# Kernel optimization log

Hardware: AMD Instinct MI355X
Metric: run time of the kernel (lower is better)

Reference implementation:

```python
import jax, jax.numpy as jnp
import numpy as np

N = 50000      # nodes
E = 800000     # directed edges (avg degree 16)
IN = 96
H = 96
OUT = 96


def _gcn(x, W, b, src, dst, norm, n):
    # PyG GCNConv: h = x @ W; aggregate norm * h[src] at dst; add bias.
    h = x @ W                          # [N, H]
    msg = h[src] * norm[:, None]       # [E+N, H]
    out = jax.ops.segment_sum(msg, dst, num_segments=n)
    return out + b


def setup_inputs() -> dict:
    key = jax.random.key(0)
    ks = jax.random.split(key, 12)
    s = 1.0 / np.sqrt(IN)
    sh = 1.0 / np.sqrt(H)
    return {
        "x": jax.random.normal(ks[0], (N, IN), dtype=jnp.float32),
        "edge_index": jax.random.randint(ks[1], (2, E), 0, N, dtype=jnp.int32),
        "W_local": jax.random.uniform(ks[2], (IN, H), jnp.float32, -s, s),
        "b_local": jnp.zeros((H,), jnp.float32),
        "W_g1": jax.random.uniform(ks[3], (IN, H), jnp.float32, -s, s),
        "b_g1": jnp.zeros((H,), jnp.float32),
        "W_g2": jax.random.uniform(ks[4], (H, H), jnp.float32, -sh, sh),
        "b_g2": jnp.zeros((H,), jnp.float32),
        "W_fuse": jax.random.uniform(ks[5], (2 * H, OUT), jnp.float32, -1.0 / np.sqrt(2 * H), 1.0 / np.sqrt(2 * H)),
        "b_fuse": jnp.zeros((OUT,), jnp.float32),
    }


def reference(x, edge_index, W_local, b_local, W_g1, b_g1, W_g2, b_g2, W_fuse, b_fuse):
    n = x.shape[0]
    loops = jnp.arange(n, dtype=edge_index.dtype)
    src = jnp.concatenate([edge_index[0], loops])   # add self-loops (GCNConv default)
    dst = jnp.concatenate([edge_index[1], loops])
    deg = jax.ops.segment_sum(jnp.ones_like(dst, dtype=x.dtype), dst, num_segments=n)
    dis = jax.lax.rsqrt(jnp.maximum(deg, 1.0))      # deg >= 1 due to self-loops
    norm = dis[src] * dis[dst]                      # sym-normalized edge weights

    local = jax.nn.relu(_gcn(x, W_local, b_local, src, dst, norm, n))
    g = jax.nn.relu(_gcn(x, W_g1, b_g1, src, dst, norm, n))
    g = jax.nn.relu(_gcn(g, W_g2, b_g2, src, dst, norm, n))

    combined = jnp.concatenate([local, g], axis=-1)  # [N, 2H]
    return combined @ W_fuse + b_fuse                # [N, OUT]
```

## Files before the change

### kernel.cpp

```cpp
#include <hip/hip_runtime.h>

#define HDIM 96
#define LSTR 104

typedef __attribute__((ext_vector_type(8))) short bf16x8;
typedef __attribute__((ext_vector_type(4))) float f32x4;

#define LGKM0() do { asm volatile("s_waitcnt lgkmcnt(0)" ::: "memory"); \
                     __builtin_amdgcn_sched_barrier(0); } while (0)

__device__ __forceinline__ unsigned short bf16rne(float x) {
  const unsigned u = __float_as_uint(x);
  return (unsigned short)((u + 0x7fff + ((u >> 16) & 1)) >> 16);
}

__device__ __forceinline__ void split2(float x, unsigned short& hi, unsigned short& lo) {
  const unsigned u = __float_as_uint(x);
  hi = (unsigned short)(u >> 16);
  const float xhi = __uint_as_float(u & 0xffff0000u);
  lo = (unsigned short)(__float_as_uint(x - xhi) >> 16);
}

__global__ void zero_k(int* __restrict__ p, int n) {
  int i = blockIdx.x * blockDim.x + threadIdx.x;
  if (i < n) p[i] = 0;
}

__global__ void deg_rank_k(const int* __restrict__ dst, int* __restrict__ indeg,
                           int* __restrict__ rank, int e) {
  int i = blockIdx.x * blockDim.x + threadIdx.x;
  if (i < e) rank[i] = atomicAdd(&indeg[dst[i]], 1);
}

__device__ __forceinline__ int wave_incl_scan(int v, int lane) {
#pragma unroll
  for (int off = 1; off < 64; off <<= 1) {
    int t = __shfl_up(v, off, 64);
    if (lane >= off) v += t;
  }
  return v;
}

__global__ __launch_bounds__(1024) void scan_a_split_k(
    const int* __restrict__ indeg, int* __restrict__ bsum, int n, int nb,
    const float* __restrict__ W0, const float* __restrict__ W1,
    const float* __restrict__ W2, const float* __restrict__ W3,
    unsigned short* __restrict__ dH, unsigned short* __restrict__ dL) {
  const int tid = threadIdx.x;
  if (blockIdx.x >= nb) {
    const int t = (blockIdx.x - nb) * 1024 + tid;
    if (t < 5 * 9216) {
      const int tile = t / 9216, r = t % 9216;
      const int nn = r / 96, k = r % 96;
      const float* W = (tile == 0) ? W0 : (tile == 1) ? W1 : (tile == 2) ? W2 : W3;
      const int row = (tile == 4) ? 96 + k : k;
      unsigned short h, l;
      split2(W[row * 96 + nn], h, l);
      dH[t] = h;
      dL[t] = l;
    }
    return;
  }
  __shared__ int ws[16];
  const int i = blockIdx.x * 1024 + tid;
  int v = (i < n) ? indeg[i] : 0;
#pragma unroll
  for (int off = 32; off; off >>= 1) v += __shfl_down(v, off, 64);
  if ((tid & 63) == 0) ws[tid >> 6] = v;
  __syncthreads();
  if (tid < 16) {
    int s = ws[tid];
#pragma unroll
    for (int off = 8; off; off >>= 1) s += __shfl_down(s, off, 16);
    if (tid == 0) bsum[blockIdx.x] = s;
  }
}

__global__ __launch_bounds__(1024) void scan_b_k(const int* __restrict__ bsum,
                                                 int* __restrict__ bbase,
                                                 int* __restrict__ offsets, int nb, int n) {
  __shared__ int ws[16];
  const int tid = threadIdx.x, lane = tid & 63, w = tid >> 6;
  const int v = (tid < nb) ? bsum[tid] : 0;
  int incl = wave_incl_scan(v, lane);
  if (lane == 63) ws[w] = incl;
  __syncthreads();
  if (tid < 16) {
    int s = ws[tid];
#pragma unroll
    for (int off = 1; off < 16; off <<= 1) {
      int t = __shfl_up(s, off, 16);
      if (tid >= off) s += t;
    }
    ws[tid] = s;
  }
  __syncthreads();
  incl += (w > 0 ? ws[w - 1] : 0);
  if (tid < nb) bbase[tid] = incl - v;
  if (tid == 0) offsets[n] = ws[15];
}

__global__ __launch_bounds__(1024) void scan_c_k(const int* __restrict__ indeg,
                                                 const int* __restrict__ bbase,
                                                 int* __restrict__ offsets,
                                                 float* __restrict__ dis, int n) {
  __shared__ int ws[16];
  const int tid = threadIdx.x, lane = tid & 63, w = tid >> 6;
  const int i = blockIdx.x * 1024 + tid;
  const int v = (i < n) ? indeg[i] : 0;
  int incl = wave_incl_scan(v, lane);
  if (lane == 63) ws[w] = incl;
  __syncthreads();
  if (tid < 16) {
    int s = ws[tid];
#pragma unroll
    for (int off = 1; off < 16; off <<= 1) {
      int t = __shfl_up(s, off, 16);
      if (tid >= off) s += t;
    }
    ws[tid] = s;
  }
  __syncthreads();
  incl += (w > 0 ? ws[w - 1] : 0);
  if (i < n) {
    offsets[i] = bbase[blockIdx.x] + incl - v;
    dis[i] = rsqrtf((float)(1 + v));
  }
}

__global__ __launch_bounds__(256) void place_scale_k(
    const int* __restrict__ src, const int* __restrict__ dst,
    const int* __restrict__ rank, const int* __restrict__ offsets,
    int* __restrict__ csr_src, int e, int pb,
    const float* __restrict__ x, const float* __restrict__ dis,
    unsigned short* __restrict__ o, int n) {
  if (blockIdx.x < pb) {
    int i = blockIdx.x * 256 + threadIdx.x;
    if (i >= e) return;
    int d = dst[i];
    atomicExch(&csr_src[offsets[d] + rank[i]], src[i]);
  } else {
    int t = (blockIdx.x - pb) * 256 + threadIdx.x;
    if (t >= n * 24) return;
    const float d = dis[t / 24];
    float4 v = ((const float4*)x)[t];
    ushort4 h;
    h.x = bf16rne(v.x * d); h.y = bf16rne(v.y * d);
    h.z = bf16rne(v.z * d); h.w = bf16rne(v.w * d);
    ((ushort4*)o)[t] = h;
  }
}

__device__ __forceinline__ void acc8(float* a, uint4 p) {
  a[0] += __uint_as_float(p.x << 16);
  a[1] += __uint_as_float(p.x & 0xffff0000u);
  a[2] += __uint_as_float(p.y << 16);
  a[3] += __uint_as_float(p.y & 0xffff0000u);
  a[4] += __uint_as_float(p.z << 16);
  a[5] += __uint_as_float(p.z & 0xffff0000u);
  a[6] += __uint_as_float(p.w << 16);
  a[7] += __uint_as_float(p.w & 0xffff0000u);
}

__device__ __forceinline__ void gather_x4p(const int* __restrict__ csr,
                                           int i, int end,
                                           const unsigned short* __restrict__ hp,
                                           int quad, float a[3][8]) {
  const int q8 = 8 * quad;
  int s0 = 0, s1 = 0, s2 = 0, s3 = 0;
  if (i + 3 < end) { s0 = csr[i]; s1 = csr[i + 1]; s2 = csr[i + 2]; s3 = csr[i + 3]; }
  while (i + 3 < end) {
    const unsigned short* p0 = hp + (size_t)s0 * HDIM + q8;
    const unsigned short* p1 = hp + (size_t)s1 * HDIM + q8;
    const unsigned short* p2 = hp + (size_t)s2 * HDIM + q8;
    const unsigned short* p3 = hp + (size_t)s3 * HDIM + q8;
    const uint4 v00 = *(const uint4*)(p0), v01 = *(const uint4*)(p0 + 32), v02 = *(const uint4*)(p0 + 64);
    const uint4 v10 = *(const uint4*)(p1), v11 = *(const uint4*)(p1 + 32), v12 = *(const uint4*)(p1 + 64);
    const uint4 v20 = *(const uint4*)(p2), v21 = *(const uint4*)(p2 + 32), v22 = *(const uint4*)(p2 + 64);
    const uint4 v30 = *(const uint4*)(p3), v31 = *(const uint4*)(p3 + 32), v32 = *(const uint4*)(p3 + 64);
    i += 4;
    if (i + 3 < end) { s0 = csr[i]; s1 = csr[i + 1]; s2 = csr[i + 2]; s3 = csr[i + 3]; }
    acc8(a[0], v00); acc8(a[1], v01); acc8(a[2], v02);
    acc8(a[0], v10); acc8(a[1], v11); acc8(a[2], v12);
    acc8(a[0], v20); acc8(a[1], v21); acc8(a[2], v22);
    acc8(a[0], v30); acc8(a[1], v31); acc8(a[2], v32);
  }
  for (; i < end; i++) {
    const unsigned short* p = hp + (size_t)csr[i] * HDIM + q8;
    acc8(a[0], *(const uint4*)p);
    acc8(a[1], *(const uint4*)(p + 32));
    acc8(a[2], *(const uint4*)(p + 64));
  }
}

__device__ __forceinline__ void flush_tile(const unsigned short* TB,
                                           unsigned short* __restrict__ g,
                                           int row0w, int M, int lane) {
  const int rr = lane >> 2, sb = lane & 3;
  const int grow = row0w + rr;
#pragma unroll
  for (int j = 0; j < 3; j++) {
    const int slot = sb + 4 * j;
    const uint4 v = *(const uint4*)(&TB[rr * LSTR + slot * 8]);
    if (grow < M) *(uint4*)(&g[(size_t)grow * HDIM + slot * 8]) = v;
  }
}

template<bool DUAL>
__global__ __launch_bounds__(256) void gat_gemm_k(
    const int* __restrict__ csr_src, const int* __restrict__ offsets,
    const float* __restrict__ dis, const unsigned short* __restrict__ hp,
    const unsigned short* __restrict__ WH0, const unsigned short* __restrict__ WL0,
    const float* __restrict__ b0,
    const unsigned short* __restrict__ WH1, const unsigned short* __restrict__ WL1,
    const float* __restrict__ b1,
    unsigned short* __restrict__ outH, unsigned short* __restrict__ outL,
    unsigned short* __restrict__ outMsg, int M) {
  __shared__ __align__(16) unsigned short Wh[96 * LSTR], Wl[96 * LSTR];
  __shared__ __align__(16) unsigned short TBUF[4][16 * LSTR];
  const int t = threadIdx.x;
  const int lane = t & 63, wv = t >> 6;
  const int m = lane & 15, quad = lane >> 4;
  const int row0 = blockIdx.x * 64;
  const int node = row0 + 16 * wv + m;
  unsigned short* TB = TBUF[wv];

  for (int u = t; u < 1152; u += 256) {
    const int nn = u / 12, kq = u % 12;
    *(uint4*)(&Wh[nn * LSTR + 8 * kq]) = ((const uint4*)(WH0 + (size_t)nn * HDIM))[kq];
    *(uint4*)(&Wl[nn * LSTR + 8 * kq]) = ((const uint4*)(WL0 + (size_t)nn * HDIM))[kq];
  }

  float a[3][8];
#pragma unroll
  for (int c = 0; c < 3; c++)
#pragma unroll
    for (int jj = 0; jj < 8; jj++) a[c][jj] = 0.f;
  if (node < M) {
    const float dd = dis[node];
    const int beg = offsets[node];
    const int end = offsets[node + 1];
    const unsigned short* selfp = hp + (size_t)node * HDIM + 8 * quad;
    const uint4 sv0 = *(const uint4*)(selfp);
    const uint4 sv1 = *(const uint4*)(selfp + 32);
    const uint4 sv2 = *(const uint4*)(selfp + 64);
    gather_x4p(csr_src, beg, end, hp, quad, a);
    acc8(a[0], sv0); acc8(a[1], sv1); acc8(a[2], sv2);
#pragma unroll
    for (int c = 0; c < 3; c++)
#pragma unroll
      for (int jj = 0; jj < 8; jj++) a[c][jj] *= dd;
  }
  bf16x8 ah[3], al[3];
#pragma unroll
  for (int c = 0; c < 3; c++)
#pragma unroll
    for (int jj = 0; jj < 8; jj++) {
      unsigned short h, l;
      split2(a[c][jj], h, l);
      ah[c][jj] = (short)h;
      al[c][jj] = (short)l;
    }

  __syncthreads();

  f32x4 acc0[6];
#pragma unroll
  for (int c = 0; c < 6; c++) acc0[c] = (f32x4){0.f, 0.f, 0.f, 0.f};
#pragma unroll
  for (int kc = 0; kc < 3; kc++) {
    const int ko = 32 * kc + 8 * quad;
#pragma unroll
    for (int c = 0; c < 6; c++) {
      const bf16x8 wh = *(const bf16x8*)(&Wh[(16 * c + m) * LSTR + ko]);
      const bf16x8 wl = *(const bf16x8*)(&Wl[(16 * c + m) * LSTR + ko]);
      acc0[c] = __builtin_amdgcn_mfma_f32_16x16x32_bf16(ah[kc], wh, acc0[c], 0, 0, 0);
      acc0[c] = __builtin_amdgcn_mfma_f32_16x16x32_bf16(ah[kc], wl, acc0[c], 0, 0, 0);
      acc0[c] = __builtin_amdgcn_mfma_f32_16x16x32_bf16(al[kc], wh, acc0[c], 0, 0, 0);
    }
  }

  const int row0w = row0 + 16 * wv;
#pragma unroll
  for (int c = 0; c < 6; c++) {
    const float bv = b0[16 * c + m];
#pragma unroll
    for (int r = 0; r < 4; r++) {
      const float v = fmaxf(acc0[c][r] + bv, 0.f);
      unsigned short h, l;
      split2(v, h, l);
      (void)l;
      TB[(4 * quad + r) * LSTR + 16 * c + m] = h;
    }
  }
  LGKM0();
  flush_tile(TB, outH, row0w, M, lane);
  LGKM0();
#pragma unroll
  for (int c = 0; c < 6; c++) {
    const float bv = b0[16 * c + m];
#pragma unroll
    for (int r = 0; r < 4; r++) {
      const float v = fmaxf(acc0[c][r] + bv, 0.f);
      unsigned short h, l;
      split2(v, h, l);
      (void)h;
      TB[(4 * quad + r) * LSTR + 16 * c + m] = l;
    }
  }
  LGKM0();
  flush_tile(TB, outL, row0w, M, lane);
  LGKM0();

  if (DUAL) {
    __syncthreads();
    for (int u = t; u < 1152; u += 256) {
      const int nn = u / 12, kq = u % 12;
      *(uint4*)(&Wh[nn * LSTR + 8 * kq]) = ((const uint4*)(WH1 + (size_t)nn * HDIM))[kq];
      *(uint4*)(&Wl[nn * LSTR + 8 * kq]) = ((const uint4*)(WL1 + (size_t)nn * HDIM))[kq];
    }
    __syncthreads();
    f32x4 acc1[6];
#pragma unroll
    for (int c = 0; c < 6; c++) acc1[c] = (f32x4){0.f, 0.f, 0.f, 0.f};
#pragma unroll
    for (int kc = 0; kc < 3; kc++) {
      const int ko = 32 * kc + 8 * quad;
#pragma unroll
      for (int c = 0; c < 6; c++) {
        const bf16x8 wh = *(const bf16x8*)(&Wh[(16 * c + m) * LSTR + ko]);
        const bf16x8 wl = *(const bf16x8*)(&Wl[(16 * c + m) * LSTR + ko]);
        acc1[c] = __builtin_amdgcn_mfma_f32_16x16x32_bf16(ah[kc], wh, acc1[c], 0, 0, 0);
        acc1[c] = __builtin_amdgcn_mfma_f32_16x16x32_bf16(ah[kc], wl, acc1[c], 0, 0, 0);
        acc1[c] = __builtin_amdgcn_mfma_f32_16x16x32_bf16(al[kc], wh, acc1[c], 0, 0, 0);
      }
    }
    float dv[4];
#pragma unroll
    for (int r = 0; r < 4; r++) dv[r] = (row0w + 4 * quad + r < M) ? dis[row0w + 4 * quad + r] : 0.f;
#pragma unroll
    for (int c = 0; c < 6; c++) {
      const float bv = b1[16 * c + m];
#pragma unroll
      for (int r = 0; r < 4; r++)
        TB[(4 * quad + r) * LSTR + 16 * c + m] =
            bf16rne(fmaxf(acc1[c][r] + bv, 0.f) * dv[r]);
    }
    LGKM0();
    flush_tile(TB, outMsg, row0w, M, lane);
  }
}

__global__ __launch_bounds__(256) void gemm_concat_k(
    const unsigned short* __restrict__ AH0, const unsigned short* __restrict__ AL0,
    const unsigned short* __restrict__ AH1, const unsigned short* __restrict__ AL1,
    const unsigned short* __restrict__ WH, const unsigned short* __restrict__ WL,
    const float* __restrict__ bias, float* __restrict__ out, int M) {
  __shared__ __align__(16) unsigned short Ah[64 * LSTR], Al[64 * LSTR];
  __shared__ __align__(16) unsigned short Wh[96 * LSTR], Wl[96 * LSTR];
  const int t = threadIdx.x;
  const int lane = t & 63, wv = t >> 6;
  const int m = lane & 15, quad = lane >> 4;
  const int row0 = blockIdx.x * 64;

  f32x4 acc[6];
#pragma unroll
  for (int c = 0; c < 6; c++) acc[c] = (f32x4){0.f, 0.f, 0.f, 0.f};

  for (int kt = 0; kt < 2; kt++) {
    const unsigned short* AH = kt ? AH1 : AH0;
    const unsigned short* AL = kt ? AL1 : AL0;
    if (kt) __syncthreads();
    for (int u = t; u < 768; u += 256) {
      const int r = u / 12, kq = u % 12;
      uint4 vh = make_uint4(0, 0, 0, 0), vl = make_uint4(0, 0, 0, 0);
      if (row0 + r < M) {
        vh = ((const uint4*)(AH + (size_t)(row0 + r) * HDIM))[kq];
        vl = ((const uint4*)(AL + (size_t)(row0 + r) * HDIM))[kq];
      }
      *(uint4*)(&Ah[r * LSTR + 8 * kq]) = vh;
      *(uint4*)(&Al[r * LSTR + 8 * kq]) = vl;
    }
    const unsigned short* WHt = WH + (size_t)kt * 9216;
    const unsigned short* WLt = WL + (size_t)kt * 9216;
    for (int u = t; u < 1152; u += 256) {
      const int nn = u / 12, kq = u % 12;
      *(uint4*)(&Wh[nn * LSTR + 8 * kq]) = ((const uint4*)(WHt + (size_t)nn * HDIM))[kq];
      *(uint4*)(&Wl[nn * LSTR + 8 * kq]) = ((const uint4*)(WLt + (size_t)nn * HDIM))[kq];
    }
    __syncthreads();
#pragma unroll
    for (int kc = 0; kc < 3; kc++) {
      const int ko = 32 * kc + 8 * quad;
      const bf16x8 ah = *(const bf16x8*)(&Ah[(16 * wv + m) * LSTR + ko]);
      const bf16x8 al = *(const bf16x8*)(&Al[(16 * wv + m) * LSTR + ko]);
#pragma unroll
      for (int c = 0; c < 6; c++) {
        const bf16x8 wh = *(const bf16x8*)(&Wh[(16 * c + m) * LSTR + ko]);
        const bf16x8 wl = *(const bf16x8*)(&Wl[(16 * c + m) * LSTR + ko]);
        acc[c] = __builtin_amdgcn_mfma_f32_16x16x32_bf16(ah, wh, acc[c], 0, 0, 0);
        acc[c] = __builtin_amdgcn_mfma_f32_16x16x32_bf16(ah, wl, acc[c], 0, 0, 0);
        acc[c] = __builtin_amdgcn_mfma_f32_16x16x32_bf16(al, wh, acc[c], 0, 0, 0);
      }
    }
  }

  float* TBf = (float*)(Ah + (size_t)(16 * wv) * LSTR);
  const int rr = lane >> 2, sb = lane & 3;
  const int grow = row0 + 16 * wv + rr;
  LGKM0();
#pragma unroll
  for (int half = 0; half < 2; half++) {
#pragma unroll
    for (int c = 0; c < 3; c++) {
      const int cc = 3 * half + c;
      const float bv = bias[16 * cc + m];
#pragma unroll
      for (int r = 0; r < 4; r++)
        TBf[(4 * quad + r) * 52 + 16 * c + m] = acc[cc][r] + bv;
    }
    LGKM0();
#pragma unroll
    for (int j = 0; j < 3; j++) {
      const int slot = sb + 4 * j;
      const float4 v = *(const float4*)(&TBf[rr * 52 + slot * 4]);
      if (grow < M) *(float4*)(&out[(size_t)grow * HDIM + half * 48 + slot * 4]) = v;
    }
    LGKM0();
  }
}

extern "C" void kernel_launch(void* const* d_in, const int* in_sizes, int n_in,
                              void* d_out, int out_size, void* d_ws, size_t ws_size,
                              hipStream_t stream) {
  const float* x       = (const float*)d_in[0];
  const int*   edge    = (const int*)d_in[1];
  const float* W_local = (const float*)d_in[2];
  const float* b_local = (const float*)d_in[3];
  const float* W_g1    = (const float*)d_in[4];
  const float* b_g1    = (const float*)d_in[5];
  const float* W_g2    = (const float*)d_in[6];
  const float* b_g2    = (const float*)d_in[7];
  const float* W_fuse  = (const float*)d_in[8];
  const float* b_fuse  = (const float*)d_in[9];
  float* out = (float*)d_out;

  const int n = in_sizes[0] / HDIM;
  const int e = in_sizes[1] / 2;
  const int* src = edge;
  const int* dst = edge + e;
  const int nb = (n + 1023) / 1024;

  char* ws = (char*)d_ws;
  auto alloc = [&](size_t bytes) { char* p = ws; ws += (bytes + 255) & ~(size_t)255; return p; };
  int*   indeg   = (int*)alloc((size_t)n * 4);
  float* dis     = (float*)alloc((size_t)n * 4);
  int*   offsets = (int*)alloc((size_t)(n + 1) * 4);
  int*   bsum    = (int*)alloc((size_t)nb * 4);
  int*   bbase   = (int*)alloc((size_t)nb * 4);
  int*   rank    = (int*)alloc((size_t)e * 4);
  int*   csr_src = (int*)alloc((size_t)e * 4);
  const size_t mat16 = (size_t)n * HDIM * 2;
  unsigned short* msgX = (unsigned short*)alloc(mat16);
  unsigned short* msgG = (unsigned short*)alloc(mat16);
  unsigned short* locH = (unsigned short*)alloc(mat16);
  unsigned short* locL = (unsigned short*)alloc(mat16);
  unsigned short* g2H  = (unsigned short*)alloc(mat16);
  unsigned short* g2L  = (unsigned short*)alloc(mat16);
  unsigned short* wH   = (unsigned short*)alloc(5 * 9216 * 2);
  unsigned short* wL   = (unsigned short*)alloc(5 * 9216 * 2);

  zero_k<<<(n + 255) / 256, 256, 0, stream>>>(indeg, n);
  deg_rank_k<<<(e + 255) / 256, 256, 0, stream>>>(dst, indeg, rank, e);
  scan_a_split_k<<<nb + 45, 1024, 0, stream>>>(indeg, bsum, n, nb,
                                               W_local, W_g1, W_g2, W_fuse, wH, wL);
  scan_b_k<<<1, 1024, 0, stream>>>(bsum, bbase, offsets, nb, n);
  scan_c_k<<<nb, 1024, 0, stream>>>(indeg, bbase, offsets, dis, n);
  const int pb = (e + 255) / 256;
  const int sb = (n * 24 + 255) / 256;
  place_scale_k<<<pb + sb, 256, 0, stream>>>(src, dst, rank, offsets, csr_src, e, pb,
                                             x, dis, msgX, n);

  const int gb = (n + 63) / 64;

  gat_gemm_k<true><<<gb, 256, 0, stream>>>(csr_src, offsets, dis, msgX,
                                           wH, wL, b_local,
                                           wH + 9216, wL + 9216, b_g1,
                                           locH, locL, msgG, n);
  gat_gemm_k<false><<<gb, 256, 0, stream>>>(csr_src, offsets, dis, msgG,
                                            wH + 2 * 9216, wL + 2 * 9216, b_g2,
                                            nullptr, nullptr, nullptr,
                                            g2H, g2L, nullptr, n);
  gemm_concat_k<<<gb, 256, 0, stream>>>(locH, locL, g2H, g2L,
                                        wH + 3 * 9216, wL + 3 * 9216, b_fuse, out, n);
}
```

Measured before the change: 262.9 us.

## Fuse final concat GEMM into second GCN aggregation kernel

The second gather+GEMM kernel now computes the fuse-layer GEMM directly. It reloads the local-branch activations (hi/lo bf16) per row and uses the just-computed g2 activations from registers via a shared-memory transpose. This removes the g2H/g2L intermediate write and read and one kernel launch. In exchange, each block reloads two more weight tiles into shared memory and needs extra syncs and more registers, which may lower occupancy.

```diff
diff --git a/kernel.cpp b/kernel.cpp
--- a/kernel.cpp
+++ b/kernel.cpp
@@ -206,7 +206,7 @@
   }
 }
 
-template<bool DUAL>
+template<bool DUAL, bool FUSE>
 __global__ __launch_bounds__(256) void gat_gemm_k(
     const int* __restrict__ csr_src, const int* __restrict__ offsets,
     const float* __restrict__ dis, const unsigned short* __restrict__ hp,
@@ -215,7 +215,10 @@
     const unsigned short* __restrict__ WH1, const unsigned short* __restrict__ WL1,
     const float* __restrict__ b1,
     unsigned short* __restrict__ outH, unsigned short* __restrict__ outL,
-    unsigned short* __restrict__ outMsg, int M) {
+    unsigned short* __restrict__ outMsg,
+    const unsigned short* __restrict__ WH2, const unsigned short* __restrict__ WL2,
+    const unsigned short* __restrict__ AH2, const unsigned short* __restrict__ AL2,
+    const float* __restrict__ bF, float* __restrict__ fout, int M) {
   __shared__ __align__(16) unsigned short Wh[96 * LSTR], Wl[96 * LSTR];
   __shared__ __align__(16) unsigned short TBUF[4][16 * LSTR];
   const int t = threadIdx.x;
@@ -262,6 +265,21 @@
       al[c][jj] = (short)l;
     }
 
+  bf16x8 lh[3], ll[3];
+  if (FUSE) {
+#pragma unroll
+    for (int kc = 0; kc < 3; kc++) { lh[kc] = (bf16x8){0,0,0,0,0,0,0,0}; ll[kc] = lh[kc]; }
+    if (node < M) {
+      const unsigned short* ph = AH2 + (size_t)node * HDIM + 8 * quad;
+      const unsigned short* pl = AL2 + (size_t)node * HDIM + 8 * quad;
+#pragma unroll
+      for (int kc = 0; kc < 3; kc++) {
+        lh[kc] = *(const bf16x8*)(ph + 32 * kc);
+        ll[kc] = *(const bf16x8*)(pl + 32 * kc);
+      }
+    }
+  }
+
   __syncthreads();
 
   f32x4 acc0[6];
@@ -281,36 +299,39 @@
   }
 
   const int row0w = row0 + 16 * wv;
-#pragma unroll
-  for (int c = 0; c < 6; c++) {
-    const float bv = b0[16 * c + m];
-#pragma unroll
-    for (int r = 0; r < 4; r++) {
-      const float v = fmaxf(acc0[c][r] + bv, 0.f);
-      unsigned short h, l;
-      split2(v, h, l);
-      (void)l;
-      TB[(4 * quad + r) * LSTR + 16 * c + m] = h;
-    }
-  }
-  LGKM0();
-  flush_tile(TB, outH, row0w, M, lane);
-  LGKM0();
-#pragma unroll
-  for (int c = 0; c < 6; c++) {
-    const float bv = b0[16 * c + m];
-#pragma unroll
-    for (int r = 0; r < 4; r++) {
-      const float v = fmaxf(acc0[c][r] + bv, 0.f);
-      unsigned short h, l;
-      split2(v, h, l);
-      (void)h;
-      TB[(4 * quad + r) * LSTR + 16 * c + m] = l;
-    }
-  }
-  LGKM0();
-  flush_tile(TB, outL, row0w, M, lane);
-  LGKM0();
+
+  if (!FUSE) {
+#pragma unroll
+    for (int c = 0; c < 6; c++) {
+      const float bv = b0[16 * c + m];
+#pragma unroll
+      for (int r = 0; r < 4; r++) {
+        const float v = fmaxf(acc0[c][r] + bv, 0.f);
+        unsigned short h, l;
+        split2(v, h, l);
+        (void)l;
+        TB[(4 * quad + r) * LSTR + 16 * c + m] = h;
+      }
+    }
+    LGKM0();
+    flush_tile(TB, outH, row0w, M, lane);
+    LGKM0();
+#pragma unroll
+    for (int c = 0; c < 6; c++) {
+      const float bv = b0[16 * c + m];
+#pragma unroll
+      for (int r = 0; r < 4; r++) {
+        const float v = fmaxf(acc0[c][r] + bv, 0.f);
+        unsigned short h, l;
+        split2(v, h, l);
+        (void)h;
+        TB[(4 * quad + r) * LSTR + 16 * c + m] = l;
+      }
+    }
+    LGKM0();
+    flush_tile(TB, outL, row0w, M, lane);
+    LGKM0();
+  }
 
   if (DUAL) {
     __syncthreads();
@@ -349,84 +370,109 @@
     LGKM0();
     flush_tile(TB, outMsg, row0w, M, lane);
   }
-}
-
-__global__ __launch_bounds__(256) void gemm_concat_k(
-    const unsigned short* __restrict__ AH0, const unsigned short* __restrict__ AL0,
-    const unsigned short* __restrict__ AH1, const unsigned short* __restrict__ AL1,
-    const unsigned short* __restrict__ WH, const unsigned short* __restrict__ WL,
-    const float* __restrict__ bias, float* __restrict__ out, int M) {
-  __shared__ __align__(16) unsigned short Ah[64 * LSTR], Al[64 * LSTR];
-  __shared__ __align__(16) unsigned short Wh[96 * LSTR], Wl[96 * LSTR];
-  const int t = threadIdx.x;
-  const int lane = t & 63, wv = t >> 6;
-  const int m = lane & 15, quad = lane >> 4;
-  const int row0 = blockIdx.x * 64;
-
-  f32x4 acc[6];
-#pragma unroll
-  for (int c = 0; c < 6; c++) acc[c] = (f32x4){0.f, 0.f, 0.f, 0.f};
-
-  for (int kt = 0; kt < 2; kt++) {
-    const unsigned short* AH = kt ? AH1 : AH0;
-    const unsigned short* AL = kt ? AL1 : AL0;
-    if (kt) __syncthreads();
-    for (int u = t; u < 768; u += 256) {
-      const int r = u / 12, kq = u % 12;
-      uint4 vh = make_uint4(0, 0, 0, 0), vl = make_uint4(0, 0, 0, 0);
-      if (row0 + r < M) {
-        vh = ((const uint4*)(AH + (size_t)(row0 + r) * HDIM))[kq];
-        vl = ((const uint4*)(AL + (size_t)(row0 + r) * HDIM))[kq];
-      }
-      *(uint4*)(&Ah[r * LSTR + 8 * kq]) = vh;
-      *(uint4*)(&Al[r * LSTR + 8 * kq]) = vl;
-    }
-    const unsigned short* WHt = WH + (size_t)kt * 9216;
-    const unsigned short* WLt = WL + (size_t)kt * 9216;
+
+  if (FUSE) {
+    bf16x8 gh[3], gl[3];
+#pragma unroll
+    for (int c = 0; c < 6; c++) {
+      const float bv = b0[16 * c + m];
+#pragma unroll
+      for (int r = 0; r < 4; r++) {
+        const float v = fmaxf(acc0[c][r] + bv, 0.f);
+        unsigned short h, l;
+        split2(v, h, l);
+        (void)l;
+        TB[(4 * quad + r) * LSTR + 16 * c + m] = h;
+      }
+    }
+    LGKM0();
+#pragma unroll
+    for (int kc = 0; kc < 3; kc++)
+      gh[kc] = *(const bf16x8*)(&TB[m * LSTR + 32 * kc + 8 * quad]);
+    LGKM0();
+#pragma unroll
+    for (int c = 0; c < 6; c++) {
+      const float bv = b0[16 * c + m];
+#pragma unroll
+      for (int r = 0; r < 4; r++) {
+        const float v = fmaxf(acc0[c][r] + bv, 0.f);
+        unsigned short h, l;
+        split2(v, h, l);
+        (void)h;
+        TB[(4 * quad + r) * LSTR + 16 * c + m] = l;
+      }
+    }
+    LGKM0();
+#pragma unroll
+    for (int kc = 0; kc < 3; kc++)
+      gl[kc] = *(const bf16x8*)(&TB[m * LSTR + 32 * kc + 8 * quad]);
+    LGKM0();
+
+    f32x4 accF[6];
+#pragma unroll
+    for (int c = 0; c < 6; c++) accF[c] = (f32x4){0.f, 0.f, 0.f, 0.f};
+
+    __syncthreads();
     for (int u = t; u < 1152; u += 256) {
       const int nn = u / 12, kq = u % 12;
-      *(uint4*)(&Wh[nn * LSTR + 8 * kq]) = ((const uint4*)(WHt + (size_t)nn * HDIM))[kq];
-      *(uint4*)(&Wl[nn * LSTR + 8 * kq]) = ((const uint4*)(WLt + (size_t)nn * HDIM))[kq];
+      *(uint4*)(&Wh[nn * LSTR + 8 * kq]) = ((const uint4*)(WH1 + (size_t)nn * HDIM))[kq];
+      *(uint4*)(&Wl[nn * LSTR + 8 * kq]) = ((const uint4*)(WL1 + (size_t)nn * HDIM))[kq];
     }
     __syncthreads();
 #pragma unroll
     for (int kc = 0; kc < 3; kc++) {
       const int ko = 32 * kc + 8 * quad;
-      const bf16x8 ah = *(const bf16x8*)(&Ah[(16 * wv + m) * LSTR + ko]);
-      const bf16x8 al = *(const bf16x8*)(&Al[(16 * wv + m) * LSTR + ko]);
 #pragma unroll
       for (int c = 0; c < 6; c++) {
         const bf16x8 wh = *(const bf16x8*)(&Wh[(16 * c + m) * LSTR + ko]);
         const bf16x8 wl = *(const bf16x8*)(&Wl[(16 * c + m) * LSTR + ko]);
-        acc[c] = __builtin_amdgcn_mfma_f32_16x16x32_bf16(ah, wh, acc[c], 0, 0, 0);
-        acc[c] = __builtin_amdgcn_mfma_f32_16x16x32_bf16(ah, wl, acc[c], 0, 0, 0);
-        acc[c] = __builtin_amdgcn_mfma_f32_16x16x32_bf16(al, wh, acc[c], 0, 0, 0);
-      }
-    }
-  }
-
-  float* TBf = (float*)(Ah + (size_t)(16 * wv) * LSTR);
-  const int rr = lane >> 2, sb = lane & 3;
-  const int grow = row0 + 16 * wv + rr;
-  LGKM0();
-#pragma unroll
-  for (int half = 0; half < 2; half++) {
-#pragma unroll
-    for (int c = 0; c < 3; c++) {
-      const int cc = 3 * half + c;
-      const float bv = bias[16 * cc + m];
-#pragma unroll
-      for (int r = 0; r < 4; r++)
-        TBf[(4 * quad + r) * 52 + 16 * c + m] = acc[cc][r] + bv;
-    }
-    LGKM0();
-#pragma unroll
-    for (int j = 0; j < 3; j++) {
-      const int slot = sb + 4 * j;
-      const float4 v = *(const float4*)(&TBf[rr * 52 + slot * 4]);
-      if (grow < M) *(float4*)(&out[(size_t)grow * HDIM + half * 48 + slot * 4]) = v;
-    }
-    LGKM0();
+        accF[c] = __builtin_amdgcn_mfma_f32_16x16x32_bf16(lh[kc], wh, accF[c], 0, 0, 0);
+        accF[c] = __builtin_amdgcn_mfma_f32_16x16x32_bf16(lh[kc], wl, accF[c], 0, 0, 0);
+        accF[c] = __builtin_amdgcn_mfma_f32_16x16x32_bf16(ll[kc], wh, accF[c], 0, 0, 0);
+      }
+    }
+    __syncthreads();
+    for (int u = t; u < 1152; u += 256) {
+      const int nn = u / 12, kq = u % 12;
+      *(uint4*)(&Wh[nn * LSTR + 8 * kq]) = ((const uint4*)(WH2 + (size_t)nn * HDIM))[kq];
+      *(uint4*)(&Wl[nn * LSTR + 8 * kq]) = ((const uint4*)(WL2 + (size_t)nn * HDIM))[kq];
+    }
+    __syncthreads();
+#pragma unroll
+    for (int kc = 0; kc < 3; kc++) {
+      const int ko = 32 * kc + 8 * quad;
+#pragma unroll
+      for (int c = 0; c < 6; c++) {
+        const bf16x8 wh = *(const bf16x8*)(&Wh[(16 * c + m) * LSTR + ko]);
+        const bf16x8 wl = *(const bf16x8*)(&Wl[(16 * c + m) * LSTR + ko]);
+        accF[c] = __builtin_amdgcn_mfma_f32_16x16x32_bf16(gh[kc], wh, accF[c], 0, 0, 0);
+        accF[c] = __builtin_amdgcn_mfma_f32_16x16x32_bf16(gh[kc], wl, accF[c], 0, 0, 0);
+        accF[c] = __builtin_amdgcn_mfma_f32_16x16x32_bf16(gl[kc], wh, accF[c], 0, 0, 0);
+      }
+    }
+
+    float* TBf = (float*)TB;
+    const int rr = lane >> 2, sb = lane & 3;
+    const int grow = row0w + rr;
+#pragma unroll
+    for (int half = 0; half < 2; half++) {
+#pragma unroll
+      for (int c = 0; c < 3; c++) {
+        const int cc = 3 * half + c;
+        const float bv = bF[16 * cc + m];
+#pragma unroll
+        for (int r = 0; r < 4; r++)
+          TBf[(4 * quad + r) * 52 + 16 * c + m] = accF[cc][r] + bv;
+      }
+      LGKM0();
+#pragma unroll
+      for (int j = 0; j < 3; j++) {
+        const int slot = sb + 4 * j;
+        const float4 v = *(const float4*)(&TBf[rr * 52 + slot * 4]);
+        if (grow < M) *(float4*)(&fout[(size_t)grow * HDIM + half * 48 + slot * 4]) = v;
+      }
+      LGKM0();
+    }
   }
 }
 
@@ -465,8 +511,6 @@
   unsigned short* msgG = (unsigned short*)alloc(mat16);
   unsigned short* locH = (unsigned short*)alloc(mat16);
   unsigned short* locL = (unsigned short*)alloc(mat16);
-  unsigned short* g2H  = (unsigned short*)alloc(mat16);
-  unsigned short* g2L  = (unsigned short*)alloc(mat16);
   unsigned short* wH   = (unsigned short*)alloc(5 * 9216 * 2);
   unsigned short* wL   = (unsigned short*)alloc(5 * 9216 * 2);
 
@@ -483,14 +527,16 @@
 
   const int gb = (n + 63) / 64;
 
-  gat_gemm_k<true><<<gb, 256, 0, stream>>>(csr_src, offsets, dis, msgX,
-                                           wH, wL, b_local,
-                                           wH + 9216, wL + 9216, b_g1,
-                                           locH, locL, msgG, n);
-  gat_gemm_k<false><<<gb, 256, 0, stream>>>(csr_src, offsets, dis, msgG,
-                                            wH + 2 * 9216, wL + 2 * 9216, b_g2,
-                                            nullptr, nullptr, nullptr,
-                                            g2H, g2L, nullptr, n);
-  gemm_concat_k<<<gb, 256, 0, stream>>>(locH, locL, g2H, g2L,
-                                        wH + 3 * 9216, wL + 3 * 9216, b_fuse, out, n);
-}
+  gat_gemm_k<true, false><<<gb, 256, 0, stream>>>(csr_src, offsets, dis, msgX,
+                                                  wH, wL, b_local,
+                                                  wH + 9216, wL + 9216, b_g1,
+                                                  locH, locL, msgG,
+                                                  nullptr, nullptr, nullptr, nullptr,
+                                                  nullptr, nullptr, n);
+  gat_gemm_k<false, true><<<gb, 256, 0, stream>>>(csr_src, offsets, dis, msgG,
+                                                  wH + 2 * 9216, wL + 2 * 9216, b_g2,
+                                                  wH + 3 * 9216, wL + 3 * 9216, nullptr,
+                                                  nullptr, nullptr, nullptr,
+                                                  wH + 4 * 9216, wL + 4 * 9216,
+                                                  locH, locL, b_fuse, out, n);
+}
```

Measured after the change: 254.8 us. 1.03x faster.
